# Kernel tuning notes

Hardware: AMD Instinct MI355X
Metric: run time of the kernel (lower is better)

The kernel has to match this reference:

```python
import jax, jax.numpy as jnp
import numpy as np

N = 50000   # nodes
E = 800000  # edges
DIN, HID, OUT = 128, 128, 64


def setup_inputs() -> dict:
    key = jax.random.key(0)
    ks = jax.random.split(key, 8)
    s = 0.05
    return {
        "x": jax.random.normal(ks[0], (N, DIN), jnp.float32),
        "edge_index": jax.random.randint(ks[1], (2, E), 0, N, dtype=jnp.int64),
        "W1": jax.random.normal(ks[2], (DIN, HID), jnp.float32) * s,
        "b1": jnp.zeros((HID,), jnp.float32),
        "W2": jax.random.normal(ks[3], (HID, OUT), jnp.float32) * s,
        "b2": jnp.zeros((OUT,), jnp.float32),
        "Wc": jax.random.normal(ks[4], (OUT, OUT), jnp.float32) * s,
        "bc": jnp.zeros((OUT,), jnp.float32),
    }


def reference(x, edge_index, W1, b1, W2, b2, Wc, bc):
    n = x.shape[0]
    src, dst = edge_index[0], edge_index[1]
    loops = jnp.arange(n, dtype=src.dtype)
    # PyG GCNConv: add self-loops, then symmetric degree normalization
    src_f = jnp.concatenate([src, loops])
    dst_f = jnp.concatenate([dst, loops])
    deg = jax.ops.segment_sum(jnp.ones(src_f.shape[0], x.dtype), dst_f, num_segments=n)
    dis = jax.lax.rsqrt(jnp.maximum(deg, 1.0))  # deg >= 1 due to self-loops
    norm = dis[src_f] * dis[dst_f]  # [E+N]

    def gcn_conv(h, W, b):
        hw = h @ W                                    # dense transform first
        msg = hw[src_f] * norm[:, None]               # gather + scale [E+N, F]
        return jax.ops.segment_sum(msg, dst_f, num_segments=n) + b

    h = jax.nn.relu(gcn_conv(x, W1, b1))
    h = gcn_conv(h, W2, b2)
    out = h @ Wc + bc
    return (h, out)
```

## Files before the change

### kernel.cpp

```cpp
#include <hip/hip_runtime.h>


#define DIN 128
#define HID 128
#define FOUT 64
#define CAP 64

using half8 = __attribute__((ext_vector_type(8))) _Float16;
using float8 = __attribute__((ext_vector_type(8))) float;
using f32x4 = __attribute__((ext_vector_type(4))) float;

__device__ inline float8 cvt8(half8 v) {
  return __builtin_convertvector(v, float8);
}

__device__ inline int part_of(int d, float invn) {
  int p = (int)((float)d * invn);
  return p > 7 ? 7 : p;
}

__global__ __launch_bounds__(256) void prep_zero_kernel(
    const float* __restrict__ W1, const float* __restrict__ W2,
    const float* __restrict__ Wc, _Float16* __restrict__ fb1,
    _Float16* __restrict__ fb2, _Float16* __restrict__ fb3,
    int* __restrict__ cnt, int N) {
  int tid = threadIdx.x;
  int i = blockIdx.x * 256 + tid;
  if (i < N) cnt[i] = 0;

  int wave = tid >> 6, lane = tid & 63;
  int m = lane & 15, quad = lane >> 4;
  if (blockIdx.x == 0) {
#pragma unroll
    for (int ct = 0; ct < 2; ++ct) {
      int n = wave * 32 + ct * 16 + m;
#pragma unroll
      for (int s = 0; s < 4; ++s) {
        half8 h;
#pragma unroll
        for (int j = 0; j < 8; ++j)
          h[j] = (_Float16)W1[(size_t)(s * 32 + quad * 8 + j) * HID + n];
        *(half8*)&fb1[((s * 2 + ct) * 256 + tid) * 8] = h;
      }
    }
  } else if (blockIdx.x == 1) {
    int n = wave * 16 + m;
#pragma unroll
    for (int s = 0; s < 4; ++s) {
      half8 h;
#pragma unroll
      for (int j = 0; j < 8; ++j)
        h[j] = (_Float16)W2[(size_t)(s * 32 + quad * 8 + j) * FOUT + n];
      *(half8*)&fb2[(s * 256 + tid) * 8] = h;
    }
  } else if (blockIdx.x == 2) {
    int n = wave * 16 + m;
#pragma unroll
    for (int s = 0; s < 2; ++s) {
      half8 h;
#pragma unroll
      for (int j = 0; j < 8; ++j)
        h[j] = (_Float16)Wc[(size_t)(s * 32 + quad * 8 + j) * FOUT + n];
      *(half8*)&fb3[(s * 256 + tid) * 8] = h;
    }
  }
}

__global__ __launch_bounds__(256) void fill_direct_kernel(
    const int* __restrict__ ei, int E, int* __restrict__ cnt,
    int* __restrict__ csr, float invn) {
  int part = blockIdx.x & 7;
  int e = (blockIdx.x >> 3) * 1024 + threadIdx.x * 4;
  if (e + 3 < E) {
    int4 d4 = *(const int4*)&ei[E + e];
    int4 s4 = *(const int4*)&ei[e];
    if (part_of(d4.x, invn) == part)
      csr[d4.x * CAP + atomicAdd(&cnt[d4.x], 1)] = s4.x;
    if (part_of(d4.y, invn) == part)
      csr[d4.y * CAP + atomicAdd(&cnt[d4.y], 1)] = s4.y;
    if (part_of(d4.z, invn) == part)
      csr[d4.z * CAP + atomicAdd(&cnt[d4.z], 1)] = s4.z;
    if (part_of(d4.w, invn) == part)
      csr[d4.w * CAP + atomicAdd(&cnt[d4.w], 1)] = s4.w;
  } else {
    for (int k = 0; k < 4; ++k) {
      if (e + k < E) {
        int d = ei[E + e + k];
        if (part_of(d, invn) == part)
          csr[d * CAP + atomicAdd(&cnt[d], 1)] = ei[e + k];
      }
    }
  }
}

__global__ __launch_bounds__(256) void gemm1_kernel(
    const float* __restrict__ x, const _Float16* __restrict__ fb1,
    const int* __restrict__ cnt, float* __restrict__ dis,
    _Float16* __restrict__ hw1, int N) {
  constexpr int KP = DIN + 8;
  __shared__ __align__(16) _Float16 As[64 * KP];
  __shared__ float disS[64];

  int tid = threadIdx.x;
  int r0 = blockIdx.x * 64;

  if (tid < 64) {
    int row = r0 + tid;
    float d = 1.0f;
    if (row < N) {
      d = rsqrtf((float)cnt[row] + 1.0f);
      dis[row] = d;
    }
    disS[tid] = d;
  }

  for (int g = tid; g < 64 * 16; g += 256) {
    int row = g >> 4, c8 = g & 15;
    half8 h = (half8)(_Float16)0;
    if (r0 + row < N) {
      const float* ap = x + (size_t)(r0 + row) * DIN + c8 * 8;
      float4 a0 = *(const float4*)ap;
      float4 a1 = *(const float4*)(ap + 4);
      h[0] = (_Float16)a0.x; h[1] = (_Float16)a0.y;
      h[2] = (_Float16)a0.z; h[3] = (_Float16)a0.w;
      h[4] = (_Float16)a1.x; h[5] = (_Float16)a1.y;
      h[6] = (_Float16)a1.z; h[7] = (_Float16)a1.w;
    }
    *(half8*)&As[row * KP + c8 * 8] = h;
  }

  int wave = tid >> 6, lane = tid & 63;
  int m = lane & 15, quad = lane >> 4;

  half8 bf[2][4];
#pragma unroll
  for (int ct = 0; ct < 2; ++ct)
#pragma unroll
    for (int s = 0; s < 4; ++s)
      bf[ct][s] = *(const half8*)&fb1[((s * 2 + ct) * 256 + tid) * 8];
  __syncthreads();

  f32x4 acc[4][2];
#pragma unroll
  for (int rt = 0; rt < 4; ++rt)
#pragma unroll
    for (int ct = 0; ct < 2; ++ct) acc[rt][ct] = (f32x4){0.f, 0.f, 0.f, 0.f};

#pragma unroll
  for (int rt = 0; rt < 4; ++rt) {
#pragma unroll
    for (int s = 0; s < 4; ++s) {
      half8 af = *(half8*)&As[(rt * 16 + m) * KP + s * 32 + quad * 8];
#pragma unroll
      for (int ct = 0; ct < 2; ++ct)
        acc[rt][ct] = __builtin_amdgcn_mfma_f32_16x16x32_f16(
            af, bf[ct][s], acc[rt][ct], 0, 0, 0);
    }
  }

#pragma unroll
  for (int rt = 0; rt < 4; ++rt) {
#pragma unroll
    for (int i = 0; i < 4; ++i) {
      int row = r0 + rt * 16 + quad * 4 + i;
      if (row >= N) continue;
      float d = disS[rt * 16 + quad * 4 + i];
#pragma unroll
      for (int ct = 0; ct < 2; ++ct)
        hw1[(size_t)row * HID + wave * 32 + ct * 16 + m] =
            (_Float16)(acc[rt][ct][i] * d);
    }
  }
}

__global__ __launch_bounds__(1024, 8) void gather1_gemm2_kernel(
    const _Float16* __restrict__ hw, const float* __restrict__ dis,
    const int* __restrict__ cnt, const int* __restrict__ csr,
    const float* __restrict__ b1, const _Float16* __restrict__ fb2,
    _Float16* __restrict__ hw2, int N) {
  constexpr int F = HID;
  constexpr int FC = F / 8;
  constexpr int EPW = 64 / FC;
  constexpr int KP = F + 8;
  __shared__ _Float16 As[16 * KP];

  int wave = threadIdx.x >> 6;
  int lane = threadIdx.x & 63;
  int eslot = lane / FC;
  int c = lane % FC;
  int n = blockIdx.x * 16 + wave;

  if (n < N) {
    const half8* hw8 = (const half8*)hw;
    float8 acc0 = {0.f, 0.f, 0.f, 0.f, 0.f, 0.f, 0.f, 0.f};
    float8 acc1 = {0.f, 0.f, 0.f, 0.f, 0.f, 0.f, 0.f, 0.f};
    if (eslot == 0)
      acc0 = cvt8(hw8[(size_t)n * FC + c]);

    int j0 = n * CAP;
    int j1 = j0 + cnt[n];
    for (int j = j0 + eslot; j < j1; j += 4 * EPW) {
      int i1 = j + EPW, i2 = j + 2 * EPW, i3 = j + 3 * EPW;
      int s0 = csr[j];
      int s1 = csr[i1 < j1 ? i1 : j];
      int s2 = csr[i2 < j1 ? i2 : j];
      int s3 = csr[i3 < j1 ? i3 : j];
      float m1 = i1 < j1 ? 1.f : 0.f;
      float m2 = i2 < j1 ? 1.f : 0.f;
      float m3 = i3 < j1 ? 1.f : 0.f;
      half8 v0 = hw8[(size_t)s0 * FC + c];
      half8 v1 = hw8[(size_t)s1 * FC + c];
      half8 v2 = hw8[(size_t)s2 * FC + c];
      half8 v3 = hw8[(size_t)s3 * FC + c];
      acc0 += cvt8(v0);
      acc1 += cvt8(v1) * m1;
      acc0 += cvt8(v2) * m2;
      acc1 += cvt8(v3) * m3;
    }
    acc0 += acc1;

#pragma unroll
    for (int st = FC; st < 64; st <<= 1) {
#pragma unroll
      for (int i = 0; i < 8; ++i) acc0[i] += __shfl_xor(acc0[i], st, 64);
    }

    if (eslot == 0) {
      float dn = dis[n];
      half8 h;
#pragma unroll
      for (int i = 0; i < 8; ++i)
        h[i] = (_Float16)fmaxf(fmaf(acc0[i], dn, b1[c * 8 + i]), 0.f);
      *(half8*)&As[wave * KP + c * 8] = h;
    }
  } else {
    if (eslot == 0) *(half8*)&As[wave * KP + c * 8] = (half8)(_Float16)0;
  }

  int m = lane & 15, quad = lane >> 4;
  half8 b[4];
  f32x4 a4 = {0.f, 0.f, 0.f, 0.f};
  int tid = threadIdx.x;
  if (wave < 4) {
#pragma unroll
    for (int s = 0; s < 4; ++s)
      b[s] = *(const half8*)&fb2[(s * 256 + tid) * 8];
  }
  __syncthreads();

  if (wave < 4) {
#pragma unroll
    for (int s = 0; s < 4; ++s) {
      half8 af = *(half8*)&As[m * KP + s * 32 + quad * 8];
      a4 = __builtin_amdgcn_mfma_f32_16x16x32_f16(af, b[s], a4, 0, 0, 0);
    }
    int nc = wave * 16 + m;
#pragma unroll
    for (int i = 0; i < 4; ++i) {
      int row = blockIdx.x * 16 + quad * 4 + i;
      if (row < N)
        hw2[(size_t)row * FOUT + nc] = (_Float16)(a4[i] * dis[row]);
    }
  }
}

__global__ __launch_bounds__(1024, 8) void gather2_head_kernel(
    const _Float16* __restrict__ hw, const float* __restrict__ dis,
    const int* __restrict__ cnt, const int* __restrict__ csr,
    const float* __restrict__ b2, const _Float16* __restrict__ fb3,
    const float* __restrict__ bc, float* __restrict__ out_h2,
    float* __restrict__ out_y, int N) {
  constexpr int F = FOUT;
  constexpr int FC = F / 8;
  constexpr int EPW = 64 / FC;
  constexpr int KP = F + 8;
  __shared__ _Float16 As[16 * KP];

  int wave = threadIdx.x >> 6;
  int lane = threadIdx.x & 63;
  int eslot = lane / FC;
  int c = lane % FC;
  int n = blockIdx.x * 16 + wave;

  if (n < N) {
    const half8* hw8 = (const half8*)hw;
    float8 acc0 = {0.f, 0.f, 0.f, 0.f, 0.f, 0.f, 0.f, 0.f};
    float8 acc1 = {0.f, 0.f, 0.f, 0.f, 0.f, 0.f, 0.f, 0.f};
    if (eslot == 0)
      acc0 = cvt8(hw8[(size_t)n * FC + c]);

    int j0 = n * CAP;
    int j1 = j0 + cnt[n];
    for (int j = j0 + eslot; j < j1; j += 4 * EPW) {
      int i1 = j + EPW, i2 = j + 2 * EPW, i3 = j + 3 * EPW;
      int s0 = csr[j];
      int s1 = csr[i1 < j1 ? i1 : j];
      int s2 = csr[i2 < j1 ? i2 : j];
      int s3 = csr[i3 < j1 ? i3 : j];
      float m1 = i1 < j1 ? 1.f : 0.f;
      float m2 = i2 < j1 ? 1.f : 0.f;
      float m3 = i3 < j1 ? 1.f : 0.f;
      half8 v0 = hw8[(size_t)s0 * FC + c];
      half8 v1 = hw8[(size_t)s1 * FC + c];
      half8 v2 = hw8[(size_t)s2 * FC + c];
      half8 v3 = hw8[(size_t)s3 * FC + c];
      acc0 += cvt8(v0);
      acc1 += cvt8(v1) * m1;
      acc0 += cvt8(v2) * m2;
      acc1 += cvt8(v3) * m3;
    }
    acc0 += acc1;

#pragma unroll
    for (int st = FC; st < 64; st <<= 1) {
#pragma unroll
      for (int i = 0; i < 8; ++i) acc0[i] += __shfl_xor(acc0[i], st, 64);
    }

    if (eslot == 0) {
      float dn = dis[n];
      float4 bb0 = *(const float4*)&b2[c * 8 + 0];
      float4 bb1 = *(const float4*)&b2[c * 8 + 4];
      float4 r0 =
          make_float4(fmaf(acc0[0], dn, bb0.x), fmaf(acc0[1], dn, bb0.y),
                      fmaf(acc0[2], dn, bb0.z), fmaf(acc0[3], dn, bb0.w));
      float4 r1 =
          make_float4(fmaf(acc0[4], dn, bb1.x), fmaf(acc0[5], dn, bb1.y),
                      fmaf(acc0[6], dn, bb1.z), fmaf(acc0[7], dn, bb1.w));
      float* op = out_h2 + (size_t)n * F + c * 8;
      *(float4*)(op + 0) = r0;
      *(float4*)(op + 4) = r1;
      half8 h;
      h[0] = (_Float16)r0.x; h[1] = (_Float16)r0.y;
      h[2] = (_Float16)r0.z; h[3] = (_Float16)r0.w;
      h[4] = (_Float16)r1.x; h[5] = (_Float16)r1.y;
      h[6] = (_Float16)r1.z; h[7] = (_Float16)r1.w;
      *(half8*)&As[wave * KP + c * 8] = h;
    }
  } else {
    if (eslot == 0) *(half8*)&As[wave * KP + c * 8] = (half8)(_Float16)0;
  }

  int m = lane & 15, quad = lane >> 4;
  half8 b[2];
  float bval = 0.f;
  f32x4 a4 = {0.f, 0.f, 0.f, 0.f};
  int tid = threadIdx.x;
  if (wave < 4) {
#pragma unroll
    for (int s = 0; s < 2; ++s)
      b[s] = *(const half8*)&fb3[(s * 256 + tid) * 8];
    bval = bc[wave * 16 + m];
  }
  __syncthreads();

  if (wave < 4) {
#pragma unroll
    for (int s = 0; s < 2; ++s) {
      half8 af = *(half8*)&As[m * KP + s * 32 + quad * 8];
      a4 = __builtin_amdgcn_mfma_f32_16x16x32_f16(af, b[s], a4, 0, 0, 0);
    }
    int nc = wave * 16 + m;
#pragma unroll
    for (int i = 0; i < 4; ++i) {
      int row = blockIdx.x * 16 + quad * 4 + i;
      if (row < N) out_y[(size_t)row * FOUT + nc] = a4[i] + bval;
    }
  }
}

extern "C" void kernel_launch(void* const* d_in, const int* in_sizes, int n_in,
                              void* d_out, int out_size, void* d_ws,
                              size_t ws_size, hipStream_t stream) {
  const float* x = (const float*)d_in[0];
  const int* ei = (const int*)d_in[1];
  const float* W1 = (const float*)d_in[2];
  const float* b1 = (const float*)d_in[3];
  const float* W2 = (const float*)d_in[4];
  const float* b2 = (const float*)d_in[5];
  const float* Wc = (const float*)d_in[6];
  const float* bc = (const float*)d_in[7];

  int N = in_sizes[0] / DIN;
  int E = in_sizes[1] / 2;
  int nper = (N + 7) / 8;
  float invn = 1.0f / (float)nper;

  char* w = (char*)d_ws;
  size_t off = 0;
  auto alloc = [&](size_t bytes) {
    char* p = w + off;
    off += (bytes + 255) & ~(size_t)255;
    return p;
  };
  int* cnt = (int*)alloc((size_t)N * 4);
  int* csr = (int*)alloc((size_t)N * CAP * 4);
  float* dis = (float*)alloc((size_t)N * 4);
  _Float16* hw1 = (_Float16*)alloc((size_t)N * DIN * 2);
  _Float16* hw2 = (_Float16*)alloc((size_t)N * FOUT * 2);
  _Float16* fb1 = (_Float16*)alloc(8 * 256 * 8 * 2);
  _Float16* fb2 = (_Float16*)alloc(4 * 256 * 8 * 2);
  _Float16* fb3 = (_Float16*)alloc(2 * 256 * 8 * 2);

  float* out_h2 = (float*)d_out;
  float* out_y = out_h2 + (size_t)N * FOUT;

  int nchunk = (E + 1023) / 1024;
  int ngrid = (N + 255) / 256;
  int ntile = (N + 63) / 64;
  int fgrid = (N + 15) / 16;

  prep_zero_kernel<<<ngrid, 256, 0, stream>>>(W1, W2, Wc, fb1, fb2, fb3, cnt,
                                              N);
  fill_direct_kernel<<<nchunk * 8, 256, 0, stream>>>(ei, E, cnt, csr, invn);
  gemm1_kernel<<<ntile, 256, 0, stream>>>(x, fb1, cnt, dis, hw1, N);

  gather1_gemm2_kernel<<<fgrid, 1024, 0, stream>>>(hw1, dis, cnt, csr, b1,
                                                   fb2, hw2, N);

  gather2_head_kernel<<<fgrid, 1024, 0, stream>>>(hw2, dis, cnt, csr, b2, fb3,
                                                  bc, out_h2, out_y, N);
}
```

Baseline: 206.0 us.

## Merge edge fill and first GEMM into one launch, recompute degree norms inline

The CSR fill and the first dense transform now run as one kernel with a split grid. Fill blocks build the adjacency and GEMM blocks compute unscaled x@W1. Because the GEMM no longer waits for degrees, the source-side normalization moves into the first gather, which loads cnt[src] per edge and recomputes rsqrt there, and the dis buffer is dropped. This removes a launch and a serialization point, but adds an extra random cnt load and rsqrt per edge in the gather.

After: 203.2 us. Within noise of the previous version (-1.3%).

```diff
diff --git a/kernel.cpp b/kernel.cpp
--- a/kernel.cpp
+++ b/kernel.cpp
@@ -66,53 +66,45 @@
   }
 }
 
-__global__ __launch_bounds__(256) void fill_direct_kernel(
-    const int* __restrict__ ei, int E, int* __restrict__ cnt,
-    int* __restrict__ csr, float invn) {
-  int part = blockIdx.x & 7;
-  int e = (blockIdx.x >> 3) * 1024 + threadIdx.x * 4;
-  if (e + 3 < E) {
-    int4 d4 = *(const int4*)&ei[E + e];
-    int4 s4 = *(const int4*)&ei[e];
-    if (part_of(d4.x, invn) == part)
-      csr[d4.x * CAP + atomicAdd(&cnt[d4.x], 1)] = s4.x;
-    if (part_of(d4.y, invn) == part)
-      csr[d4.y * CAP + atomicAdd(&cnt[d4.y], 1)] = s4.y;
-    if (part_of(d4.z, invn) == part)
-      csr[d4.z * CAP + atomicAdd(&cnt[d4.z], 1)] = s4.z;
-    if (part_of(d4.w, invn) == part)
-      csr[d4.w * CAP + atomicAdd(&cnt[d4.w], 1)] = s4.w;
-  } else {
-    for (int k = 0; k < 4; ++k) {
-      if (e + k < E) {
-        int d = ei[E + e + k];
-        if (part_of(d, invn) == part)
-          csr[d * CAP + atomicAdd(&cnt[d], 1)] = ei[e + k];
+__global__ __launch_bounds__(256) void fill_gemm1_kernel(
+    const int* __restrict__ ei, int E, int N, const float* __restrict__ x,
+    const _Float16* __restrict__ fb1, int* __restrict__ cnt,
+    int* __restrict__ csr, _Float16* __restrict__ hw1, float invn,
+    int nfill) {
+  __shared__ __align__(16) _Float16 As[64 * (DIN + 8)];
+  int tid = threadIdx.x;
+  int bid = blockIdx.x;
+
+  if (bid < nfill) {
+    int part = bid & 7;
+    int e = (bid >> 3) * 1024 + tid * 4;
+    if (e + 3 < E) {
+      int4 d4 = *(const int4*)&ei[E + e];
+      int4 s4 = *(const int4*)&ei[e];
+      if (part_of(d4.x, invn) == part)
+        csr[d4.x * CAP + atomicAdd(&cnt[d4.x], 1)] = s4.x;
+      if (part_of(d4.y, invn) == part)
+        csr[d4.y * CAP + atomicAdd(&cnt[d4.y], 1)] = s4.y;
+      if (part_of(d4.z, invn) == part)
+        csr[d4.z * CAP + atomicAdd(&cnt[d4.z], 1)] = s4.z;
+      if (part_of(d4.w, invn) == part)
+        csr[d4.w * CAP + atomicAdd(&cnt[d4.w], 1)] = s4.w;
+    } else {
+      for (int k = 0; k < 4; ++k) {
+        if (e + k < E) {
+          int d = ei[E + e + k];
+          if (part_of(d, invn) == part)
+            csr[d * CAP + atomicAdd(&cnt[d], 1)] = ei[e + k];
+        }
       }
     }
-  }
-}
-
-__global__ __launch_bounds__(256) void gemm1_kernel(
-    const float* __restrict__ x, const _Float16* __restrict__ fb1,
-    const int* __restrict__ cnt, float* __restrict__ dis,
-    _Float16* __restrict__ hw1, int N) {
+    return;
+  }
+
   constexpr int KP = DIN + 8;
-  __shared__ __align__(16) _Float16 As[64 * KP];
-  __shared__ float disS[64];
-
-  int tid = threadIdx.x;
-  int r0 = blockIdx.x * 64;
-
-  if (tid < 64) {
-    int row = r0 + tid;
-    float d = 1.0f;
-    if (row < N) {
-      d = rsqrtf((float)cnt[row] + 1.0f);
-      dis[row] = d;
-    }
-    disS[tid] = d;
-  }
+  int r0 = (bid - nfill) * 64;
+  int wave = tid >> 6, lane = tid & 63;
+  int m = lane & 15, quad = lane >> 4;
 
   for (int g = tid; g < 64 * 16; g += 256) {
     int row = g >> 4, c8 = g & 15;
@@ -129,9 +121,6 @@
     *(half8*)&As[row * KP + c8 * 8] = h;
   }
 
-  int wave = tid >> 6, lane = tid & 63;
-  int m = lane & 15, quad = lane >> 4;
-
   half8 bf[2][4];
 #pragma unroll
   for (int ct = 0; ct < 2; ++ct)
@@ -164,20 +153,18 @@
     for (int i = 0; i < 4; ++i) {
       int row = r0 + rt * 16 + quad * 4 + i;
       if (row >= N) continue;
-      float d = disS[rt * 16 + quad * 4 + i];
 #pragma unroll
       for (int ct = 0; ct < 2; ++ct)
         hw1[(size_t)row * HID + wave * 32 + ct * 16 + m] =
-            (_Float16)(acc[rt][ct][i] * d);
+            (_Float16)acc[rt][ct][i];
     }
   }
 }
 
 __global__ __launch_bounds__(1024, 8) void gather1_gemm2_kernel(
-    const _Float16* __restrict__ hw, const float* __restrict__ dis,
-    const int* __restrict__ cnt, const int* __restrict__ csr,
-    const float* __restrict__ b1, const _Float16* __restrict__ fb2,
-    _Float16* __restrict__ hw2, int N) {
+    const _Float16* __restrict__ hw, const int* __restrict__ cnt,
+    const int* __restrict__ csr, const float* __restrict__ b1,
+    const _Float16* __restrict__ fb2, _Float16* __restrict__ hw2, int N) {
   constexpr int F = HID;
   constexpr int FC = F / 8;
   constexpr int EPW = 64 / FC;
@@ -192,13 +179,113 @@
 
   if (n < N) {
     const half8* hw8 = (const half8*)hw;
+    int deg = cnt[n];
+    float dn = rsqrtf((float)deg + 1.0f);
+    float8 acc0 = {0.f, 0.f, 0.f, 0.f, 0.f, 0.f, 0.f, 0.f};
+    float8 acc1 = {0.f, 0.f, 0.f, 0.f, 0.f, 0.f, 0.f, 0.f};
+    if (eslot == 0)
+      acc0 = cvt8(hw8[(size_t)n * FC + c]) * dn;
+
+    int j0 = n * CAP;
+    int j1 = j0 + deg;
+    for (int j = j0 + eslot; j < j1; j += 4 * EPW) {
+      int i1 = j + EPW, i2 = j + 2 * EPW, i3 = j + 3 * EPW;
+      int s0 = csr[j];
+      int s1 = csr[i1 < j1 ? i1 : j];
+      int s2 = csr[i2 < j1 ? i2 : j];
+      int s3 = csr[i3 < j1 ? i3 : j];
+      int c0 = cnt[s0];
+      int c1 = cnt[s1];
+      int c2 = cnt[s2];
+      int c3 = cnt[s3];
+      half8 v0 = hw8[(size_t)s0 * FC + c];
+      half8 v1 = hw8[(size_t)s1 * FC + c];
+      half8 v2 = hw8[(size_t)s2 * FC + c];
+      half8 v3 = hw8[(size_t)s3 * FC + c];
+      float d0 = rsqrtf((float)c0 + 1.0f);
+      float d1 = (i1 < j1 ? 1.f : 0.f) * rsqrtf((float)c1 + 1.0f);
+      float d2 = (i2 < j1 ? 1.f : 0.f) * rsqrtf((float)c2 + 1.0f);
+      float d3 = (i3 < j1 ? 1.f : 0.f) * rsqrtf((float)c3 + 1.0f);
+      acc0 += cvt8(v0) * d0;
+      acc1 += cvt8(v1) * d1;
+      acc0 += cvt8(v2) * d2;
+      acc1 += cvt8(v3) * d3;
+    }
+    acc0 += acc1;
+
+#pragma unroll
+    for (int st = FC; st < 64; st <<= 1) {
+#pragma unroll
+      for (int i = 0; i < 8; ++i) acc0[i] += __shfl_xor(acc0[i], st, 64);
+    }
+
+    if (eslot == 0) {
+      half8 h;
+#pragma unroll
+      for (int i = 0; i < 8; ++i)
+        h[i] = (_Float16)fmaxf(fmaf(acc0[i], dn, b1[c * 8 + i]), 0.f);
+      *(half8*)&As[wave * KP + c * 8] = h;
+    }
+  } else {
+    if (eslot == 0) *(half8*)&As[wave * KP + c * 8] = (half8)(_Float16)0;
+  }
+
+  int m = lane & 15, quad = lane >> 4;
+  half8 b[4];
+  f32x4 a4 = {0.f, 0.f, 0.f, 0.f};
+  int tid = threadIdx.x;
+  if (wave < 4) {
+#pragma unroll
+    for (int s = 0; s < 4; ++s)
+      b[s] = *(const half8*)&fb2[(s * 256 + tid) * 8];
+  }
+  __syncthreads();
+
+  if (wave < 4) {
+#pragma unroll
+    for (int s = 0; s < 4; ++s) {
+      half8 af = *(half8*)&As[m * KP + s * 32 + quad * 8];
+      a4 = __builtin_amdgcn_mfma_f32_16x16x32_f16(af, b[s], a4, 0, 0, 0);
+    }
+    int nc = wave * 16 + m;
+#pragma unroll
+    for (int i = 0; i < 4; ++i) {
+      int row = blockIdx.x * 16 + quad * 4 + i;
+      if (row < N) {
+        float dr = rsqrtf((float)cnt[row] + 1.0f);
+        hw2[(size_t)row * FOUT + nc] = (_Float16)(a4[i] * dr);
+      }
+    }
+  }
+}
+
+__global__ __launch_bounds__(1024, 8) void gather2_head_kernel(
+    const _Float16* __restrict__ hw, const int* __restrict__ cnt,
+    const int* __restrict__ csr, const float* __restrict__ b2,
+    const _Float16* __restrict__ fb3, const float* __restrict__ bc,
+    float* __restrict__ out_h2, float* __restrict__ out_y, int N) {
+  constexpr int F = FOUT;
+  constexpr int FC = F / 8;
+  constexpr int EPW = 64 / FC;
+  constexpr int KP = F + 8;
+  __shared__ _Float16 As[16 * KP];
+
+  int wave = threadIdx.x >> 6;
+  int lane = threadIdx.x & 63;
+  int eslot = lane / FC;
+  int c = lane % FC;
+  int n = blockIdx.x * 16 + wave;
+
+  if (n < N) {
+    const half8* hw8 = (const half8*)hw;
+    int deg = cnt[n];
     float8 acc0 = {0.f, 0.f, 0.f, 0.f, 0.f, 0.f, 0.f, 0.f};
     float8 acc1 = {0.f, 0.f, 0.f, 0.f, 0.f, 0.f, 0.f, 0.f};
     if (eslot == 0)
       acc0 = cvt8(hw8[(size_t)n * FC + c]);
 
     int j0 = n * CAP;
-    int j1 = j0 + cnt[n];
+    int j1 = j0 + deg;
     for (int j = j0 + eslot; j < j1; j += 4 * EPW) {
       int i1 = j + EPW, i2 = j + 2 * EPW, i3 = j + 3 * EPW;
       int s0 = csr[j];
@@ -226,99 +313,7 @@
     }
 
     if (eslot == 0) {
-      float dn = dis[n];
-      half8 h;
-#pragma unroll
-      for (int i = 0; i < 8; ++i)
-        h[i] = (_Float16)fmaxf(fmaf(acc0[i], dn, b1[c * 8 + i]), 0.f);
-      *(half8*)&As[wave * KP + c * 8] = h;
-    }
-  } else {
-    if (eslot == 0) *(half8*)&As[wave * KP + c * 8] = (half8)(_Float16)0;
-  }
-
-  int m = lane & 15, quad = lane >> 4;
-  half8 b[4];
-  f32x4 a4 = {0.f, 0.f, 0.f, 0.f};
-  int tid = threadIdx.x;
-  if (wave < 4) {
-#pragma unroll
-    for (int s = 0; s < 4; ++s)
-      b[s] = *(const half8*)&fb2[(s * 256 + tid) * 8];
-  }
-  __syncthreads();
-
-  if (wave < 4) {
-#pragma unroll
-    for (int s = 0; s < 4; ++s) {
-      half8 af = *(half8*)&As[m * KP + s * 32 + quad * 8];
-      a4 = __builtin_amdgcn_mfma_f32_16x16x32_f16(af, b[s], a4, 0, 0, 0);
-    }
-    int nc = wave * 16 + m;
-#pragma unroll
-    for (int i = 0; i < 4; ++i) {
-      int row = blockIdx.x * 16 + quad * 4 + i;
-      if (row < N)
-        hw2[(size_t)row * FOUT + nc] = (_Float16)(a4[i] * dis[row]);
-    }
-  }
-}
-
-__global__ __launch_bounds__(1024, 8) void gather2_head_kernel(
-    const _Float16* __restrict__ hw, const float* __restrict__ dis,
-    const int* __restrict__ cnt, const int* __restrict__ csr,
-    const float* __restrict__ b2, const _Float16* __restrict__ fb3,
-    const float* __restrict__ bc, float* __restrict__ out_h2,
-    float* __restrict__ out_y, int N) {
-  constexpr int F = FOUT;
-  constexpr int FC = F / 8;
-  constexpr int EPW = 64 / FC;
-  constexpr int KP = F + 8;
-  __shared__ _Float16 As[16 * KP];
-
-  int wave = threadIdx.x >> 6;
-  int lane = threadIdx.x & 63;
-  int eslot = lane / FC;
-  int c = lane % FC;
-  int n = blockIdx.x * 16 + wave;
-
-  if (n < N) {
-    const half8* hw8 = (const half8*)hw;
-    float8 acc0 = {0.f, 0.f, 0.f, 0.f, 0.f, 0.f, 0.f, 0.f};
-    float8 acc1 = {0.f, 0.f, 0.f, 0.f, 0.f, 0.f, 0.f, 0.f};
-    if (eslot == 0)
-      acc0 = cvt8(hw8[(size_t)n * FC + c]);
-
-    int j0 = n * CAP;
-    int j1 = j0 + cnt[n];
-    for (int j = j0 + eslot; j < j1; j += 4 * EPW) {
-      int i1 = j + EPW, i2 = j + 2 * EPW, i3 = j + 3 * EPW;
-      int s0 = csr[j];
-      int s1 = csr[i1 < j1 ? i1 : j];
-      int s2 = csr[i2 < j1 ? i2 : j];
-      int s3 = csr[i3 < j1 ? i3 : j];
-      float m1 = i1 < j1 ? 1.f : 0.f;
-      float m2 = i2 < j1 ? 1.f : 0.f;
-      float m3 = i3 < j1 ? 1.f : 0.f;
-      half8 v0 = hw8[(size_t)s0 * FC + c];
-      half8 v1 = hw8[(size_t)s1 * FC + c];
-      half8 v2 = hw8[(size_t)s2 * FC + c];
-      half8 v3 = hw8[(size_t)s3 * FC + c];
-      acc0 += cvt8(v0);
-      acc1 += cvt8(v1) * m1;
-      acc0 += cvt8(v2) * m2;
-      acc1 += cvt8(v3) * m3;
-    }
-    acc0 += acc1;
-
-#pragma unroll
-    for (int st = FC; st < 64; st <<= 1) {
-#pragma unroll
-      for (int i = 0; i < 8; ++i) acc0[i] += __shfl_xor(acc0[i], st, 64);
-    }
-
-    if (eslot == 0) {
-      float dn = dis[n];
+      float dn = rsqrtf((float)deg + 1.0f);
       float4 bb0 = *(const float4*)&b2[c * 8 + 0];
       float4 bb1 = *(const float4*)&b2[c * 8 + 4];
       float4 r0 =
@@ -395,7 +390,6 @@
   };
   int* cnt = (int*)alloc((size_t)N * 4);
   int* csr = (int*)alloc((size_t)N * CAP * 4);
-  float* dis = (float*)alloc((size_t)N * 4);
   _Float16* hw1 = (_Float16*)alloc((size_t)N * DIN * 2);
   _Float16* hw2 = (_Float16*)alloc((size_t)N * FOUT * 2);
   _Float16* fb1 = (_Float16*)alloc(8 * 256 * 8 * 2);
@@ -409,15 +403,16 @@
   int ngrid = (N + 255) / 256;
   int ntile = (N + 63) / 64;
   int fgrid = (N + 15) / 16;
+  int nfill = nchunk * 8;
 
   prep_zero_kernel<<<ngrid, 256, 0, stream>>>(W1, W2, Wc, fb1, fb2, fb3, cnt,
                                               N);
-  fill_direct_kernel<<<nchunk * 8, 256, 0, stream>>>(ei, E, cnt, csr, invn);
-  gemm1_kernel<<<ntile, 256, 0, stream>>>(x, fb1, cnt, dis, hw1, N);
-
-  gather1_gemm2_kernel<<<fgrid, 1024, 0, stream>>>(hw1, dis, cnt, csr, b1,
-                                                   fb2, hw2, N);
-
-  gather2_head_kernel<<<fgrid, 1024, 0, stream>>>(hw2, dis, cnt, csr, b2, fb3,
-                                                  bc, out_h2, out_y, N);
-}
+  fill_gemm1_kernel<<<nfill + ntile, 256, 0, stream>>>(
+      ei, E, N, x, fb1, cnt, csr, hw1, invn, nfill);
+
+  gather1_gemm2_kernel<<<fgrid, 1024, 0, stream>>>(hw1, cnt, csr, b1, fb2,
+                                                   hw2, N);
+
+  gather2_head_kernel<<<fgrid, 1024, 0, stream>>>(hw2, cnt, csr, b2, fb3, bc,
+                                                  out_h2, out_y, N);
+}
```
